# Kernel optimization log

Hardware: AMD Instinct MI355X
Metric: run time of the kernel (lower is better)

Reference implementation:

```python
import jax, jax.numpy as jnp
import numpy as np

BETA = 0.25

def setup_inputs() -> dict:
    key = jax.random.key(0)
    k1, k2 = jax.random.split(key)
    x = jax.random.normal(k1, (16, 256, 32, 32), dtype=jnp.float32)
    emb_weight = jax.random.normal(k2, (8192, 256), dtype=jnp.float32) * 0.02
    return {"x": x, "emb_weight": emb_weight}

def reference(x, emb_weight):
    # b c h w -> b h w c
    xt = jnp.transpose(x, (0, 2, 3, 1))
    D = emb_weight.shape[1]
    xf = xt.reshape(-1, D)  # [N, D]
    # squared euclidean distances: [N, K]
    dist = (jnp.sum(xf * xf, axis=1, keepdims=True)
            + jnp.sum(emb_weight * emb_weight, axis=1)
            - 2.0 * xf @ emb_weight.T)
    indices = jnp.argmin(dist, axis=1)  # [N]
    x_q = emb_weight[indices].reshape(xt.shape)  # [B,H,W,D]
    sg = jax.lax.stop_gradient
    loss = (BETA * jnp.mean(jnp.square(sg(x_q) - xt))
            + jnp.mean(jnp.square(x_q - sg(xt))))
    # straight-through estimator
    x_q_st = xt + sg(x_q - xt)
    out = jnp.transpose(x_q_st, (0, 3, 1, 2))  # b h w c -> b c h w
    return out, loss, indices
```

## Files before the change

### kernel.cpp

```cpp
#include <hip/hip_runtime.h>

#define NPTS   16384
#define KCODES 8192
#define DDIM   256
#define HWSZ   1024
#define CHW    (DDIM * HWSZ)
#define OUT_ELEMS 4194304
#define LOSS_OFF  OUT_ELEMS
#define IDX_OFF   (OUT_ELEMS + 1)

#define PTB   64
#define CTILE 128
#define KC    64
#define NIT   256
#define XPITCH 264

typedef _Float16 half_t;
typedef __attribute__((ext_vector_type(8))) _Float16 half8;
typedef __attribute__((ext_vector_type(4))) float     v4f;

union HU { _Float16 h; unsigned short u; };

#define EHI_WORDS  (256 * 8192)
#define SE_OFF_B   (2 * EHI_WORDS * 2)

#define GLD16(gp, lp) __builtin_amdgcn_global_load_lds( \
    (const __attribute__((address_space(1))) unsigned int*)(gp), \
    (__attribute__((address_space(3))) unsigned int*)(lp), 16, 0, 0)

__global__ void prep_kernel(const float* __restrict__ emb,
                            unsigned short* __restrict__ ehi,
                            unsigned short* __restrict__ elo,
                            float* __restrict__ se)
{
    const int gw   = (blockIdx.x * 256 + threadIdx.x) >> 6;
    const int lane = threadIdx.x & 63;
    for (int i = 0; i < 8; ++i) {
        const int c = gw * 8 + i;
        const float4 v = *(const float4*)(emb + (size_t)c * DDIM + lane * 4);
        float ps = v.x * v.x;
        ps = fmaf(v.y, v.y, ps); ps = fmaf(v.z, v.z, ps); ps = fmaf(v.w, v.w, ps);
        float tot = ps;
        #pragma unroll
        for (int off = 1; off < 64; off <<= 1) tot += __shfl_xor(tot, off);
        if (lane == 0) se[c] = tot;
        const float E0 = v.x * 64.f, E1 = v.y * 64.f, E2 = v.z * 64.f, E3 = v.w * 64.f;
        const half_t h0 = (half_t)E0, h1 = (half_t)E1, h2 = (half_t)E2, h3 = (half_t)E3;
        const half_t l0 = (half_t)((E0 - (float)h0) * 2048.f);
        const half_t l1 = (half_t)((E1 - (float)h1) * 2048.f);
        const half_t l2 = (half_t)((E2 - (float)h2) * 2048.f);
        const half_t l3 = (half_t)((E3 - (float)h3) * 2048.f);
        HU a0, a1, a2, a3, b0, b1, b2, b3;
        a0.h = h0; a1.h = h1; a2.h = h2; a3.h = h3;
        b0.h = l0; b1.h = l1; b2.h = l2; b3.h = l3;
        const unsigned int uh0 = (unsigned)a0.u | ((unsigned)a1.u << 16);
        const unsigned int uh1 = (unsigned)a2.u | ((unsigned)a3.u << 16);
        const unsigned int ul0 = (unsigned)b0.u | ((unsigned)b1.u << 16);
        const unsigned int ul1 = (unsigned)b2.u | ((unsigned)b3.u << 16);
        const int ck = lane >> 4;
        const int kb = (lane & 15) >> 1;
        const int hf = lane & 1;
        const int T = c >> 7, r = c & 127;
        const size_t base = (((size_t)(T * 4 + ck) * 128 + r) * 64)
                          + (size_t)((kb ^ (r & 7)) * 8) + hf * 4;
        *(unsigned int*)&ehi[base]     = uh0;
        *(unsigned int*)&ehi[base + 2] = uh1;
        *(unsigned int*)&elo[base]     = ul0;
        *(unsigned int*)&elo[base + 2] = ul1;
    }
}

__launch_bounds__(512)
__global__ void vq_kernel(const float* __restrict__ x,
                          const unsigned short* __restrict__ ehi,
                          const unsigned short* __restrict__ elo,
                          const float* __restrict__ wse,
                          const float* __restrict__ emb,
                          float* __restrict__ out)
{
    __shared__ __align__(16) unsigned short ldsXH[PTB][XPITCH];
    __shared__ __align__(16) unsigned short ldsXL[PTB][XPITCH];
    __shared__ __align__(16) unsigned short ldsEH[2][8192];
    __shared__ __align__(16) unsigned short ldsEL[2][8192];
    __shared__ float  ldsRS[8][65];
    __shared__ float  ldsS[PTB];
    __shared__ float  ldsFD[8][32];
    __shared__ int    ldsFI[8][32];
    __shared__ int    ldsI[PTB];
    __shared__ double ldsL[8];

    const int t    = threadIdx.x;
    const int lane = t & 63;
    const int w    = t >> 6;
    const int n0   = blockIdx.x * PTB;
    const int b    = n0 / HWSZ;
    const int hw0  = n0 % HWSZ;
    const float* xs = x + (size_t)b * CHW + hw0;

    const int part = (w & 3) * 4096;
    #define STAGE(img, buf) do { \
        const char* _g = (const char*)((w < 4) ? ehi : elo) \
                       + (size_t)(img) * 16384 + part + lane * 16; \
        char* _l = (char*)((w < 4) ? ldsEH[buf] : ldsEL[buf]) + part; \
        GLD16(_g,          _l); \
        GLD16(_g + 1024,   _l + 1024); \
        GLD16(_g + 2048,   _l + 2048); \
        GLD16(_g + 3072,   _l + 3072); \
    } while (0)

    STAGE(0, 0);

    {
        const int p   = t & 63;
        const int seg = t >> 6;
        float a = 0.f;
        for (int i = 0; i < 32; ++i) {
            const int c = seg * 32 + i;
            const float v = xs[(size_t)c * HWSZ + p];
            const half_t hh = (half_t)v;
            const half_t hl = (half_t)((v - (float)hh) * 2048.0f);
            HU u0; u0.h = hh; ldsXH[p][c] = u0.u;
            HU u1; u1.h = hl; ldsXL[p][c] = u1.u;
            a = fmaf(v, v, a);
        }
        ldsRS[seg][p] = a;
    }
    __syncthreads();
    if (t < PTB) {
        float s = 0.f;
        for (int g = 0; g < 8; ++g) s += ldsRS[g][t];
        ldsS[t] = s;
    }
    __syncthreads();

    const int h32 = (w & 1) * 32;
    const int q32 = (w >> 1) * 32;
    const int ln  = lane & 15;
    const int qd  = lane >> 4;

    float s_frag[8];
    #pragma unroll
    for (int pbi = 0; pbi < 2; ++pbi)
        #pragma unroll
        for (int r = 0; r < 4; ++r)
            s_frag[pbi * 4 + r] = ldsS[h32 + pbi * 16 + qd * 4 + r];

    float best_d[8]; int best_i[8];
    #pragma unroll
    for (int i = 0; i < 8; ++i) { best_d[i] = 3.4e38f; best_i[i] = 0; }

    v4f acc_hh[2][2], acc_hl[2][2];
    float se0 = 0.f, se1 = 0.f;

    for (int it = 0; it < NIT; ++it) {
        const int ck  = it & 3;
        const int buf = it & 1;
        if (ck == 0) {
            #pragma unroll
            for (int i = 0; i < 2; ++i)
                #pragma unroll
                for (int j = 0; j < 2; ++j)
                    #pragma unroll
                    for (int r = 0; r < 4; ++r) { acc_hh[i][j][r] = 0.f; acc_hl[i][j][r] = 0.f; }
        }
        __syncthreads();
        if (it + 1 < NIT) STAGE(it + 1, (it + 1) & 1);
        if (ck == 2) {
            const int tb2 = (it >> 2) * CTILE;
            se0 = wse[tb2 + q32 + ln];
            se1 = wse[tb2 + q32 + 16 + ln];
        }
        #pragma unroll
        for (int kk = 0; kk < 2; ++kk) {
            const int ka  = ck * KC + kk * 32 + qd * 8;
            const int swz = ((kk * 4 + qd) ^ (ln & 7)) * 8;
            const int rL  = (q32 + ln) * 64;
            const int rH  = (q32 + 16 + ln) * 64;
            const half8 ah0 = *(const half8*)&ldsXH[h32 + ln][ka];
            const half8 ah1 = *(const half8*)&ldsXH[h32 + 16 + ln][ka];
            const half8 al0 = *(const half8*)&ldsXL[h32 + ln][ka];
            const half8 al1 = *(const half8*)&ldsXL[h32 + 16 + ln][ka];
            const half8 bh0 = *(const half8*)&ldsEH[buf][rL + swz];
            const half8 bh1 = *(const half8*)&ldsEH[buf][rH + swz];
            const half8 bl0 = *(const half8*)&ldsEL[buf][rL + swz];
            const half8 bl1 = *(const half8*)&ldsEL[buf][rH + swz];
            acc_hh[0][0] = __builtin_amdgcn_mfma_f32_16x16x32_f16(ah0, bh0, acc_hh[0][0], 0, 0, 0);
            acc_hh[0][1] = __builtin_amdgcn_mfma_f32_16x16x32_f16(ah0, bh1, acc_hh[0][1], 0, 0, 0);
            acc_hh[1][0] = __builtin_amdgcn_mfma_f32_16x16x32_f16(ah1, bh0, acc_hh[1][0], 0, 0, 0);
            acc_hh[1][1] = __builtin_amdgcn_mfma_f32_16x16x32_f16(ah1, bh1, acc_hh[1][1], 0, 0, 0);
            acc_hl[0][0] = __builtin_amdgcn_mfma_f32_16x16x32_f16(ah0, bl0, acc_hl[0][0], 0, 0, 0);
            acc_hl[0][1] = __builtin_amdgcn_mfma_f32_16x16x32_f16(ah0, bl1, acc_hl[0][1], 0, 0, 0);
            acc_hl[1][0] = __builtin_amdgcn_mfma_f32_16x16x32_f16(ah1, bl0, acc_hl[1][0], 0, 0, 0);
            acc_hl[1][1] = __builtin_amdgcn_mfma_f32_16x16x32_f16(ah1, bl1, acc_hl[1][1], 0, 0, 0);
            acc_hl[0][0] = __builtin_amdgcn_mfma_f32_16x16x32_f16(al0, bh0, acc_hl[0][0], 0, 0, 0);
            acc_hl[0][1] = __builtin_amdgcn_mfma_f32_16x16x32_f16(al0, bh1, acc_hl[0][1], 0, 0, 0);
            acc_hl[1][0] = __builtin_amdgcn_mfma_f32_16x16x32_f16(al1, bh0, acc_hl[1][0], 0, 0, 0);
            acc_hl[1][1] = __builtin_amdgcn_mfma_f32_16x16x32_f16(al1, bh1, acc_hl[1][1], 0, 0, 0);
        }
        if (ck == 3) {
            const int tb = (it >> 2) * CTILE;
            #pragma unroll
            for (int csi = 0; csi < 2; ++csi) {
                const float se   = csi ? se1 : se0;
                const int   code = tb + q32 + csi * 16 + ln;
                #pragma unroll
                for (int pbi = 0; pbi < 2; ++pbi)
                    #pragma unroll
                    for (int r = 0; r < 4; ++r) {
                        const float m  = fmaf(acc_hl[pbi][csi][r], 4.8828125e-4f,
                                              acc_hh[pbi][csi][r]) * 0.015625f;
                        const float T  = s_frag[pbi * 4 + r] + se;
                        const float dd = fmaf(-2.0f, m, T);
                        const int   s  = pbi * 4 + r;
                        if (dd < best_d[s]) { best_d[s] = dd; best_i[s] = code; }
                    }
            }
        }
    }

    #pragma unroll
    for (int off = 1; off < 16; off <<= 1) {
        #pragma unroll
        for (int s = 0; s < 8; ++s) {
            const float d2 = __shfl_xor(best_d[s], off);
            const int   i2 = __shfl_xor(best_i[s], off);
            if (d2 < best_d[s] || (d2 == best_d[s] && i2 < best_i[s])) {
                best_d[s] = d2; best_i[s] = i2;
            }
        }
    }
    if (ln == 0) {
        #pragma unroll
        for (int pbi = 0; pbi < 2; ++pbi)
            #pragma unroll
            for (int r = 0; r < 4; ++r) {
                ldsFD[w][pbi * 16 + qd * 4 + r] = best_d[pbi * 4 + r];
                ldsFI[w][pbi * 16 + qd * 4 + r] = best_i[pbi * 4 + r];
            }
    }
    __syncthreads();
    if (t < PTB) {
        const int hh  = t >> 5;
        const int r32 = t & 31;
        float bd = 3.4e38f; int bi = 0;
        #pragma unroll
        for (int qq = 0; qq < 4; ++qq) {
            const int wv = hh + qq * 2;
            const float d2 = ldsFD[wv][r32];
            const int   i2 = ldsFI[wv][r32];
            if (d2 < bd || (d2 == bd && i2 < bi)) { bd = d2; bi = i2; }
        }
        ldsI[t] = bi;
        out[(size_t)IDX_OFF + n0 + t] = (float)bi;
    }
    __syncthreads();

    double lsum = 0.0;
    {
        const int p  = t & 63;
        const int cg = t >> 6;
        const int row = ldsI[p];
        const float* erow = emb + (size_t)row * DDIM;
        float* ob = out + (size_t)b * CHW + hw0 + p;
        for (int q = 0; q < 32; ++q) {
            const int c = cg * 32 + q;
            const float e  = erow[c];
            const float xx = xs[(size_t)c * HWSZ + p];
            const float diff = e - xx;
            ob[(size_t)c * HWSZ] = xx + diff;
            lsum += (double)diff * (double)diff;
        }
    }
    #pragma unroll
    for (int off = 32; off > 0; off >>= 1)
        lsum += __shfl_xor(lsum, off);
    if ((t & 63) == 0) ldsL[t >> 6] = lsum;
    __syncthreads();
    if (t == 0) {
        double tot = 0.0;
        #pragma unroll
        for (int wv = 0; wv < 8; ++wv) tot += ldsL[wv];
        atomicAdd(&out[LOSS_OFF], (float)(tot * (1.25 / 4194304.0)));
    }
}

extern "C" void kernel_launch(void* const* d_in, const int* in_sizes, int n_in,
                              void* d_out, int out_size, void* d_ws, size_t ws_size,
                              hipStream_t stream) {
    (void)in_sizes; (void)n_in; (void)out_size; (void)ws_size;
    const float* x   = (const float*)d_in[0];
    const float* emb = (const float*)d_in[1];
    float* out = (float*)d_out;
    unsigned short* ehi = (unsigned short*)d_ws;
    unsigned short* elo = ehi + EHI_WORDS;
    float*          wse = (float*)((char*)d_ws + SE_OFF_B);
    hipMemsetAsync((char*)d_out + (size_t)LOSS_OFF * sizeof(float), 0, sizeof(float), stream);
    prep_kernel<<<256, 256, 0, stream>>>(emb, ehi, elo, wse);
    vq_kernel<<<NPTS / PTB, 512, 0, stream>>>(x, ehi, elo, wse, emb, out);
}
```

Before: 318.9 us.

## Keep x fragments in registers and switch to 32x32x16 MFMA tiles

Each wave now loads its 32 points' hi/lo fp16 split of x directly into registers (16 half8 pairs each) instead of staging x through LDS, so only the codebook B operand is read from LDS. The wave tiling changes to 2 point groups by 4 code groups, using 32x32x16 MFMA with one v16f accumulator pair, which halves B-fragment LDS reads per FLOP. The hi and lo codebook halves are interleaved into one image per stage, so a single double-buffered LDS array is used. The cost is heavy register pressure from the x fragments, which may lower occupancy or cause spills, plus a redundant wraparound prefetch on the last stage.

Measured after the change: 346.2 us. +8.5%, slower.

```diff
diff --git a/kernel.cpp b/kernel.cpp
--- a/kernel.cpp
+++ b/kernel.cpp
@@ -9,28 +9,24 @@
 #define LOSS_OFF  OUT_ELEMS
 #define IDX_OFF   (OUT_ELEMS + 1)
 
-#define PTB   64
-#define CTILE 128
-#define KC    64
-#define NIT   256
-#define XPITCH 264
+#define PTB    64
+#define NTILE  64
+#define IMG_US 16384
+#define IMG_B  32768
+#define SE_OFF_B (256 * IMG_B)
 
 typedef _Float16 half_t;
-typedef __attribute__((ext_vector_type(8))) _Float16 half8;
-typedef __attribute__((ext_vector_type(4))) float     v4f;
+typedef __attribute__((ext_vector_type(8)))  _Float16 half8;
+typedef __attribute__((ext_vector_type(16))) float    v16f;
 
 union HU { _Float16 h; unsigned short u; };
-
-#define EHI_WORDS  (256 * 8192)
-#define SE_OFF_B   (2 * EHI_WORDS * 2)
 
 #define GLD16(gp, lp) __builtin_amdgcn_global_load_lds( \
     (const __attribute__((address_space(1))) unsigned int*)(gp), \
     (__attribute__((address_space(3))) unsigned int*)(lp), 16, 0, 0)
 
 __global__ void prep_kernel(const float* __restrict__ emb,
-                            unsigned short* __restrict__ ehi,
-                            unsigned short* __restrict__ elo,
+                            unsigned short* __restrict__ eimg,
                             float* __restrict__ se)
 {
     const int gw   = (blockIdx.x * 256 + threadIdx.x) >> 6;
@@ -50,39 +46,34 @@
         const half_t l1 = (half_t)((E1 - (float)h1) * 2048.f);
         const half_t l2 = (half_t)((E2 - (float)h2) * 2048.f);
         const half_t l3 = (half_t)((E3 - (float)h3) * 2048.f);
-        HU a0, a1, a2, a3, b0, b1, b2, b3;
-        a0.h = h0; a1.h = h1; a2.h = h2; a3.h = h3;
-        b0.h = l0; b1.h = l1; b2.h = l2; b3.h = l3;
-        const unsigned int uh0 = (unsigned)a0.u | ((unsigned)a1.u << 16);
-        const unsigned int uh1 = (unsigned)a2.u | ((unsigned)a3.u << 16);
-        const unsigned int ul0 = (unsigned)b0.u | ((unsigned)b1.u << 16);
-        const unsigned int ul1 = (unsigned)b2.u | ((unsigned)b3.u << 16);
-        const int ck = lane >> 4;
-        const int kb = (lane & 15) >> 1;
-        const int hf = lane & 1;
-        const int T = c >> 7, r = c & 127;
-        const size_t base = (((size_t)(T * 4 + ck) * 128 + r) * 64)
-                          + (size_t)((kb ^ (r & 7)) * 8) + hf * 4;
-        *(unsigned int*)&ehi[base]     = uh0;
-        *(unsigned int*)&ehi[base + 2] = uh1;
-        *(unsigned int*)&elo[base]     = ul0;
-        *(unsigned int*)&elo[base + 2] = ul1;
+        HU uha, uhb, uhc, uhd, ula, ulb, ulc, uld;
+        uha.h = h0; uhb.h = h1; uhc.h = h2; uhd.h = h3;
+        ula.h = l0; ulb.h = l1; ulc.h = l2; uld.h = l3;
+        const unsigned int wh0 = (unsigned)uha.u | ((unsigned)uhb.u << 16);
+        const unsigned int wh1 = (unsigned)uhc.u | ((unsigned)uhd.u << 16);
+        const unsigned int wl0 = (unsigned)ula.u | ((unsigned)ulb.u << 16);
+        const unsigned int wl1 = (unsigned)ulc.u | ((unsigned)uld.u << 16);
+        const int kl  = lane * 4;
+        const int img = (c >> 7) * 4 + (kl >> 6);
+        const int k64 = kl & 63;
+        const int r   = c & 127;
+        const int blk = (k64 >> 3) ^ (r & 7);
+        const size_t base = (size_t)img * IMG_US + r * 64 + blk * 8 + (k64 & 7);
+        *(unsigned int*)&eimg[base]            = wh0;
+        *(unsigned int*)&eimg[base + 2]        = wh1;
+        *(unsigned int*)&eimg[base + 8192]     = wl0;
+        *(unsigned int*)&eimg[base + 8192 + 2] = wl1;
     }
 }
 
 __launch_bounds__(512)
 __global__ void vq_kernel(const float* __restrict__ x,
-                          const unsigned short* __restrict__ ehi,
-                          const unsigned short* __restrict__ elo,
+                          const unsigned short* __restrict__ eimg,
                           const float* __restrict__ wse,
                           const float* __restrict__ emb,
                           float* __restrict__ out)
 {
-    __shared__ __align__(16) unsigned short ldsXH[PTB][XPITCH];
-    __shared__ __align__(16) unsigned short ldsXL[PTB][XPITCH];
-    __shared__ __align__(16) unsigned short ldsEH[2][8192];
-    __shared__ __align__(16) unsigned short ldsEL[2][8192];
-    __shared__ float  ldsRS[8][65];
+    __shared__ __align__(16) unsigned short ldsE[2][IMG_US];
     __shared__ float  ldsS[PTB];
     __shared__ float  ldsFD[8][32];
     __shared__ int    ldsFI[8][32];
@@ -92,162 +83,125 @@
     const int t    = threadIdx.x;
     const int lane = t & 63;
     const int w    = t >> 6;
+    const int pg   = w >> 2;
+    const int cg   = w & 3;
     const int n0   = blockIdx.x * PTB;
     const int b    = n0 / HWSZ;
     const int hw0  = n0 % HWSZ;
     const float* xs = x + (size_t)b * CHW + hw0;
 
-    const int part = (w & 3) * 4096;
     #define STAGE(img, buf) do { \
-        const char* _g = (const char*)((w < 4) ? ehi : elo) \
-                       + (size_t)(img) * 16384 + part + lane * 16; \
-        char* _l = (char*)((w < 4) ? ldsEH[buf] : ldsEL[buf]) + part; \
-        GLD16(_g,          _l); \
-        GLD16(_g + 1024,   _l + 1024); \
-        GLD16(_g + 2048,   _l + 2048); \
-        GLD16(_g + 3072,   _l + 3072); \
+        const char* _g = (const char*)eimg + (size_t)(img) * IMG_B + w * 4096 + lane * 16; \
+        char* _l = (char*)ldsE[buf] + w * 4096; \
+        GLD16(_g,        _l); \
+        GLD16(_g + 1024, _l + 1024); \
+        GLD16(_g + 2048, _l + 2048); \
+        GLD16(_g + 3072, _l + 3072); \
     } while (0)
 
     STAGE(0, 0);
 
-    {
-        const int p   = t & 63;
-        const int seg = t >> 6;
-        float a = 0.f;
-        for (int i = 0; i < 32; ++i) {
-            const int c = seg * 32 + i;
-            const float v = xs[(size_t)c * HWSZ + p];
+    const int prow  = pg * 32 + (lane & 31);
+    const int khalf = (lane >> 5) * 8;
+    const float* xp = xs + prow;
+    half8 xh[16], xl[16];
+    float sq = 0.f;
+    #pragma unroll
+    for (int xc = 0; xc < 16; ++xc) {
+        #pragma unroll
+        for (int j = 0; j < 8; ++j) {
+            const int c = xc * 16 + khalf + j;
+            const float v = xp[(size_t)c * HWSZ];
             const half_t hh = (half_t)v;
             const half_t hl = (half_t)((v - (float)hh) * 2048.0f);
-            HU u0; u0.h = hh; ldsXH[p][c] = u0.u;
-            HU u1; u1.h = hl; ldsXL[p][c] = u1.u;
-            a = fmaf(v, v, a);
-        }
-        ldsRS[seg][p] = a;
+            xh[xc][j] = hh;
+            xl[xc][j] = hl;
+            sq = fmaf(v, v, sq);
+        }
+    }
+    const float s_p = sq + __shfl_xor(sq, 32);
+    if ((w == 0 || w == 4) && (lane & 63) < 32) ldsS[pg * 32 + lane] = s_p;
+    __syncthreads();
+
+    float s_frag[16];
+    #pragma unroll
+    for (int q = 0; q < 16; ++q) {
+        const int rl = (q & 3) + 8 * (q >> 2) + 4 * (lane >> 5);
+        s_frag[q] = ldsS[pg * 32 + rl];
+    }
+
+    float best_d[16]; int best_i[16];
+    #pragma unroll
+    for (int q = 0; q < 16; ++q) { best_d[q] = 3.4e38f; best_i[q] = 0; }
+
+    const int rr  = cg * 32 + (lane & 31);
+    const int rb7 = rr & 7;
+    float se_reg = 0.f;
+    v16f acc_hh, acc_hl;
+
+    for (int tile = 0; tile < NTILE; ++tile) {
+        #pragma unroll
+        for (int q = 0; q < 16; ++q) { acc_hh[q] = 0.f; acc_hl[q] = 0.f; }
+        #pragma unroll
+        for (int kc = 0; kc < 4; ++kc) {
+            const int buf = kc & 1;
+            __syncthreads();
+            {
+                int nimg = tile * 4 + kc + 1;
+                if (nimg == 256) nimg = 0;
+                STAGE(nimg, (kc + 1) & 1);
+            }
+            if (kc == 2) se_reg = wse[tile * 128 + rr];
+            #pragma unroll
+            for (int s = 0; s < 4; ++s) {
+                const int bblk = (s * 2 + (lane >> 5)) ^ rb7;
+                const unsigned short* bp = &ldsE[buf][rr * 64 + bblk * 8];
+                const half8 bh = *(const half8*)bp;
+                const half8 bl = *(const half8*)(bp + 8192);
+                const int xc = kc * 4 + s;
+                acc_hh = __builtin_amdgcn_mfma_f32_32x32x16_f16(xh[xc], bh, acc_hh, 0, 0, 0);
+                acc_hl = __builtin_amdgcn_mfma_f32_32x32x16_f16(xh[xc], bl, acc_hl, 0, 0, 0);
+                acc_hl = __builtin_amdgcn_mfma_f32_32x32x16_f16(xl[xc], bh, acc_hl, 0, 0, 0);
+            }
+        }
+        const int code = tile * 128 + rr;
+        #pragma unroll
+        for (int q = 0; q < 16; ++q) {
+            const float m = fmaf(acc_hl[q], 4.8828125e-4f, acc_hh[q]) * 0.015625f;
+            const float T = s_frag[q] + se_reg;
+            const float d = fmaf(-2.0f, m, T);
+            if (d < best_d[q]) { best_d[q] = d; best_i[q] = code; }
+        }
+    }
+
+    #pragma unroll
+    for (int off = 1; off < 32; off <<= 1) {
+        #pragma unroll
+        for (int q = 0; q < 16; ++q) {
+            const float d2 = __shfl_xor(best_d[q], off);
+            const int   i2 = __shfl_xor(best_i[q], off);
+            if (d2 < best_d[q] || (d2 == best_d[q] && i2 < best_i[q])) {
+                best_d[q] = d2; best_i[q] = i2;
+            }
+        }
+    }
+    if ((lane & 31) == 0) {
+        #pragma unroll
+        for (int q = 0; q < 16; ++q) {
+            const int rl = (q & 3) + 8 * (q >> 2) + 4 * (lane >> 5);
+            ldsFD[w][rl] = best_d[q];
+            ldsFI[w][rl] = best_i[q];
+        }
     }
     __syncthreads();
     if (t < PTB) {
-        float s = 0.f;
-        for (int g = 0; g < 8; ++g) s += ldsRS[g][t];
-        ldsS[t] = s;
-    }
-    __syncthreads();
-
-    const int h32 = (w & 1) * 32;
-    const int q32 = (w >> 1) * 32;
-    const int ln  = lane & 15;
-    const int qd  = lane >> 4;
-
-    float s_frag[8];
-    #pragma unroll
-    for (int pbi = 0; pbi < 2; ++pbi)
-        #pragma unroll
-        for (int r = 0; r < 4; ++r)
-            s_frag[pbi * 4 + r] = ldsS[h32 + pbi * 16 + qd * 4 + r];
-
-    float best_d[8]; int best_i[8];
-    #pragma unroll
-    for (int i = 0; i < 8; ++i) { best_d[i] = 3.4e38f; best_i[i] = 0; }
-
-    v4f acc_hh[2][2], acc_hl[2][2];
-    float se0 = 0.f, se1 = 0.f;
-
-    for (int it = 0; it < NIT; ++it) {
-        const int ck  = it & 3;
-        const int buf = it & 1;
-        if (ck == 0) {
-            #pragma unroll
-            for (int i = 0; i < 2; ++i)
-                #pragma unroll
-                for (int j = 0; j < 2; ++j)
-                    #pragma unroll
-                    for (int r = 0; r < 4; ++r) { acc_hh[i][j][r] = 0.f; acc_hl[i][j][r] = 0.f; }
-        }
-        __syncthreads();
-        if (it + 1 < NIT) STAGE(it + 1, (it + 1) & 1);
-        if (ck == 2) {
-            const int tb2 = (it >> 2) * CTILE;
-            se0 = wse[tb2 + q32 + ln];
-            se1 = wse[tb2 + q32 + 16 + ln];
-        }
-        #pragma unroll
-        for (int kk = 0; kk < 2; ++kk) {
-            const int ka  = ck * KC + kk * 32 + qd * 8;
-            const int swz = ((kk * 4 + qd) ^ (ln & 7)) * 8;
-            const int rL  = (q32 + ln) * 64;
-            const int rH  = (q32 + 16 + ln) * 64;
-            const half8 ah0 = *(const half8*)&ldsXH[h32 + ln][ka];
-            const half8 ah1 = *(const half8*)&ldsXH[h32 + 16 + ln][ka];
-            const half8 al0 = *(const half8*)&ldsXL[h32 + ln][ka];
-            const half8 al1 = *(const half8*)&ldsXL[h32 + 16 + ln][ka];
-            const half8 bh0 = *(const half8*)&ldsEH[buf][rL + swz];
-            const half8 bh1 = *(const half8*)&ldsEH[buf][rH + swz];
-            const half8 bl0 = *(const half8*)&ldsEL[buf][rL + swz];
-            const half8 bl1 = *(const half8*)&ldsEL[buf][rH + swz];
-            acc_hh[0][0] = __builtin_amdgcn_mfma_f32_16x16x32_f16(ah0, bh0, acc_hh[0][0], 0, 0, 0);
-            acc_hh[0][1] = __builtin_amdgcn_mfma_f32_16x16x32_f16(ah0, bh1, acc_hh[0][1], 0, 0, 0);
-            acc_hh[1][0] = __builtin_amdgcn_mfma_f32_16x16x32_f16(ah1, bh0, acc_hh[1][0], 0, 0, 0);
-            acc_hh[1][1] = __builtin_amdgcn_mfma_f32_16x16x32_f16(ah1, bh1, acc_hh[1][1], 0, 0, 0);
-            acc_hl[0][0] = __builtin_amdgcn_mfma_f32_16x16x32_f16(ah0, bl0, acc_hl[0][0], 0, 0, 0);
-            acc_hl[0][1] = __builtin_amdgcn_mfma_f32_16x16x32_f16(ah0, bl1, acc_hl[0][1], 0, 0, 0);
-            acc_hl[1][0] = __builtin_amdgcn_mfma_f32_16x16x32_f16(ah1, bl0, acc_hl[1][0], 0, 0, 0);
-            acc_hl[1][1] = __builtin_amdgcn_mfma_f32_16x16x32_f16(ah1, bl1, acc_hl[1][1], 0, 0, 0);
-            acc_hl[0][0] = __builtin_amdgcn_mfma_f32_16x16x32_f16(al0, bh0, acc_hl[0][0], 0, 0, 0);
-            acc_hl[0][1] = __builtin_amdgcn_mfma_f32_16x16x32_f16(al0, bh1, acc_hl[0][1], 0, 0, 0);
-            acc_hl[1][0] = __builtin_amdgcn_mfma_f32_16x16x32_f16(al1, bh0, acc_hl[1][0], 0, 0, 0);
-            acc_hl[1][1] = __builtin_amdgcn_mfma_f32_16x16x32_f16(al1, bh1, acc_hl[1][1], 0, 0, 0);
-        }
-        if (ck == 3) {
-            const int tb = (it >> 2) * CTILE;
-            #pragma unroll
-            for (int csi = 0; csi < 2; ++csi) {
-                const float se   = csi ? se1 : se0;
-                const int   code = tb + q32 + csi * 16 + ln;
-                #pragma unroll
-                for (int pbi = 0; pbi < 2; ++pbi)
-                    #pragma unroll
-                    for (int r = 0; r < 4; ++r) {
-                        const float m  = fmaf(acc_hl[pbi][csi][r], 4.8828125e-4f,
-                                              acc_hh[pbi][csi][r]) * 0.015625f;
-                        const float T  = s_frag[pbi * 4 + r] + se;
-                        const float dd = fmaf(-2.0f, m, T);
-                        const int   s  = pbi * 4 + r;
-                        if (dd < best_d[s]) { best_d[s] = dd; best_i[s] = code; }
-                    }
-            }
-        }
-    }
-
-    #pragma unroll
-    for (int off = 1; off < 16; off <<= 1) {
-        #pragma unroll
-        for (int s = 0; s < 8; ++s) {
-            const float d2 = __shfl_xor(best_d[s], off);
-            const int   i2 = __shfl_xor(best_i[s], off);
-            if (d2 < best_d[s] || (d2 == best_d[s] && i2 < best_i[s])) {
-                best_d[s] = d2; best_i[s] = i2;
-            }
-        }
-    }
-    if (ln == 0) {
-        #pragma unroll
-        for (int pbi = 0; pbi < 2; ++pbi)
-            #pragma unroll
-            for (int r = 0; r < 4; ++r) {
-                ldsFD[w][pbi * 16 + qd * 4 + r] = best_d[pbi * 4 + r];
-                ldsFI[w][pbi * 16 + qd * 4 + r] = best_i[pbi * 4 + r];
-            }
-    }
-    __syncthreads();
-    if (t < PTB) {
-        const int hh  = t >> 5;
-        const int r32 = t & 31;
-        float bd = 3.4e38f; int bi = 0;
-        #pragma unroll
-        for (int qq = 0; qq < 4; ++qq) {
-            const int wv = hh + qq * 2;
-            const float d2 = ldsFD[wv][r32];
-            const int   i2 = ldsFI[wv][r32];
+        const int pg2 = t >> 5, rl = t & 31;
+        float bd = ldsFD[pg2 * 4][rl];
+        int   bi = ldsFI[pg2 * 4][rl];
+        #pragma unroll
+        for (int c2 = 1; c2 < 4; ++c2) {
+            const float d2 = ldsFD[pg2 * 4 + c2][rl];
+            const int   i2 = ldsFI[pg2 * 4 + c2][rl];
             if (d2 < bd || (d2 == bd && i2 < bi)) { bd = d2; bi = i2; }
         }
         ldsI[t] = bi;
@@ -258,12 +212,12 @@
     double lsum = 0.0;
     {
         const int p  = t & 63;
-        const int cg = t >> 6;
+        const int cgp = t >> 6;
         const int row = ldsI[p];
         const float* erow = emb + (size_t)row * DDIM;
         float* ob = out + (size_t)b * CHW + hw0 + p;
         for (int q = 0; q < 32; ++q) {
-            const int c = cg * 32 + q;
+            const int c = cgp * 32 + q;
             const float e  = erow[c];
             const float xx = xs[(size_t)c * HWSZ + p];
             const float diff = e - xx;
@@ -291,10 +245,9 @@
     const float* x   = (const float*)d_in[0];
     const float* emb = (const float*)d_in[1];
     float* out = (float*)d_out;
-    unsigned short* ehi = (unsigned short*)d_ws;
-    unsigned short* elo = ehi + EHI_WORDS;
-    float*          wse = (float*)((char*)d_ws + SE_OFF_B);
-    hipMemsetAsync((char*)d_out + (size_t)LOSS_OFF * sizeof(float), 0, sizeof(float), stream);
-    prep_kernel<<<256, 256, 0, stream>>>(emb, ehi, elo, wse);
-    vq_kernel<<<NPTS / PTB, 512, 0, stream>>>(x, ehi, elo, wse, emb, out);
+    unsigned short* eimg = (unsigned short*)d_ws;
+    float*          wse  = (float*)((char*)d_ws + SE_OFF_B);
+    (void)hipMemsetAsync((char*)d_out + (size_t)LOSS_OFF * sizeof(float), 0, sizeof(float), stream);
+    prep_kernel<<<256, 256, 0, stream>>>(emb, eimg, wse);
+    vq_kernel<<<NPTS / PTB, 512, 0, stream>>>(x, eimg, wse, emb, out);
 }
```
